# Kernel tuning notes

Hardware: AMD Instinct MI355X
Metric: run time of the kernel (lower is better)

The kernel has to match this reference:

```python
import jax, jax.numpy as jnp
import numpy as np

E = 256      # emb_size
H = 100      # ff_sim hidden
B, TQ, TK = 16, 128, 128


def setup_inputs() -> dict:
    key = jax.random.key(0)
    ks = jax.random.split(key, 8)
    queries = jax.random.normal(ks[0], (B, TQ, E), dtype=jnp.float32)
    keys = jax.random.normal(ks[1], (B, TK, E), dtype=jnp.float32)
    query_masks = jnp.ones((B, TQ), dtype=jnp.float32)
    key_masks = jnp.ones((B, TK), dtype=jnp.float32)
    # xavier_uniform bounds: sqrt(6/(fan_in+fan_out))
    def xavier(k, shape):
        fan_out, fan_in = shape
        lim = np.sqrt(6.0 / (fan_in + fan_out))
        return jax.random.uniform(k, shape, jnp.float32, -lim, lim)
    W1 = xavier(ks[2], (H, 2 * E))          # linear_ff_sim[0].weight
    b1 = jnp.zeros((H,), dtype=jnp.float32)  # linear_ff_sim[0].bias
    W2 = xavier(ks[3], (1, H))              # linear_ff_sim[2].weight (no bias)
    Wlast = xavier(ks[4], (E, 2 * E))       # linear_last.weight
    blast = jnp.zeros((E,), dtype=jnp.float32)
    return {"queries": queries, "keys": keys, "query_masks": query_masks,
            "key_masks": key_masks, "W1": W1, "b1": b1, "W2": W2,
            "Wlast": Wlast, "blast": blast}


def reference(queries, keys, query_masks, key_masks, W1, b1, W2, Wlast, blast):
    # forward calls attention_fc(keys, queries, key_masks, query_masks):
    #   attn queries = keys,  attn keys = queries,
    #   attn query_masks = key_masks, attn key_masks = query_masks.
    e = queries.shape[-1]
    # Additive-attention MLP score, decomposed: cat([keys_i, queries_j]) @ W1^T
    #   = keys_i @ W1[:, :E]^T + queries_j @ W1[:, E:]^T
    a = jnp.einsum('bie,he->bih', keys, W1[:, :e])      # [B,Tk,H]
    c = jnp.einsum('bje,he->bjh', queries, W1[:, e:])   # [B,Tq,H]
    h = jnp.tanh(a[:, :, None, :] + c[:, None, :, :] + b1)  # [B,Tk,Tq,H]
    sim = jnp.einsum('bijh,h->bij', h, W2[0])           # [B,Tk,Tq]
    neg = jnp.asarray(-2.0 ** 32 + 1, sim.dtype)
    sim = jnp.where(query_masks[:, None, :] == 0, neg, sim)
    sim = jax.nn.softmax(sim, axis=-1)
    sim = sim * key_masks[:, :, None]
    keys_attn = jnp.einsum('bij,bje->bie', sim, queries)  # [B,Tk,E]
    feature_mul = keys_attn * keys
    d = keys_attn - keys
    feature_sub = d * d
    feature_last = jnp.concatenate([feature_mul, feature_sub], axis=-1)  # [B,Tk,2E]
    return jax.nn.relu(jnp.einsum('bif,ef->bie', feature_last, Wlast) + blast)
```

## Files before the change

### kernel.cpp

```cpp
#include <hip/hip_runtime.h>


namespace {
constexpr int B  = 16;
constexpr int TQ = 128;
constexpr int TK = 128;
constexpr int E  = 256;
constexpr int H  = 100;
constexpr int HP = 112;
constexpr int G  = 4;
}

typedef __attribute__((ext_vector_type(8))) short short8;
typedef __attribute__((ext_vector_type(4))) float f32x4;

__device__ __forceinline__ unsigned short f2bf(float f) {
  unsigned u = __builtin_bit_cast(unsigned, f);
  u = (u + 0x7FFFu + ((u >> 16) & 1u)) >> 16;
  return (unsigned short)u;
}

__global__ __launch_bounds__(256) void convert_bf16(
    const float* __restrict__ queries, const float* __restrict__ keys,
    const float* __restrict__ W1, const float* __restrict__ Wlast,
    unsigned short* __restrict__ Xb, unsigned short* __restrict__ Wb1,
    unsigned short* __restrict__ Wb) {
  const int blk = blockIdx.x, t = threadIdx.x;
  if (blk < 1024) {
    const int idx = blk * 1024 + t * 4;
    const int row = idx >> 8, e = idx & 255;
    const float* src = (row < B * TK) ? keys + (size_t)row * E + e
                                      : queries + (size_t)(row - B * TK) * E + e;
    float4 v = *(const float4*)src;
    ushort4 o = make_ushort4(f2bf(v.x), f2bf(v.y), f2bf(v.z), f2bf(v.w));
    *(ushort4*)(Xb + idx) = o;
  } else if (blk < 1080) {
    const int idx = (blk - 1024) * 1024 + t * 4;
    const int h = idx >> 9;
    float4 v = (h < H) ? *(const float4*)(W1 + idx)
                       : make_float4(0.f, 0.f, 0.f, 0.f);
    ushort4 o = make_ushort4(f2bf(v.x), f2bf(v.y), f2bf(v.z), f2bf(v.w));
    *(ushort4*)(Wb1 + idx) = o;
  } else {
    const int idx = (blk - 1080) * 1024 + t * 4;
    float4 v = *(const float4*)(Wlast + idx);
    ushort4 o = make_ushort4(f2bf(v.x), f2bf(v.y), f2bf(v.z), f2bf(v.w));
    *(ushort4*)(Wb + idx) = o;
  }
}

__global__ __launch_bounds__(256) void prep_mfma(
    const unsigned short* __restrict__ Xb, const unsigned short* __restrict__ Wb1,
    const float* __restrict__ b1, float* __restrict__ A, float* __restrict__ C) {
  __shared__ short Bs[112 * 264];
  __shared__ short As[16 * 264];
  const int t  = threadIdx.x;
  const int m0 = blockIdx.x * 16;
  const bool isA = (m0 < B * TK);
  const int koff = isA ? 0 : 256;
  float* dst = isA ? (A + (size_t)m0 * HP)
                   : (C + (size_t)(m0 - B * TK) * HP);

  #pragma unroll
  for (int i = 0; i < 14; ++i) {
    const int idx = i * 256 + t;
    const int h = idx >> 5, seg = idx & 31;
    *(uint4*)(Bs + h * 264 + seg * 8) =
        *(const uint4*)(Wb1 + (size_t)h * 512 + koff + seg * 8);
  }
  #pragma unroll
  for (int i = 0; i < 2; ++i) {
    const int idx = i * 256 + t;
    const int r = idx >> 5, seg = idx & 31;
    *(uint4*)(As + r * 264 + seg * 8) =
        *(const uint4*)(Xb + (size_t)(m0 + r) * 256 + seg * 8);
  }
  __syncthreads();

  const int wave = t >> 6, lane = t & 63;
  const int m = lane & 15, kq = lane >> 4;
  const int nt0 = wave, nt1 = wave + 4;
  f32x4 acc0 = {0.f, 0.f, 0.f, 0.f}, acc1 = {0.f, 0.f, 0.f, 0.f};

  #pragma unroll
  for (int kc = 0; kc < 8; ++kc) {
    short8 a = *(const short8*)(As + m * 264 + kc * 32 + kq * 8);
    short8 bv0 = *(const short8*)(Bs + (nt0 * 16 + m) * 264 + kc * 32 + kq * 8);
    acc0 = __builtin_amdgcn_mfma_f32_16x16x32_bf16(a, bv0, acc0, 0, 0, 0);
    if (nt1 < 7) {
      short8 bv1 = *(const short8*)(Bs + (nt1 * 16 + m) * 264 + kc * 32 + kq * 8);
      acc1 = __builtin_amdgcn_mfma_f32_16x16x32_bf16(a, bv1, acc1, 0, 0, 0);
    }
  }

  const int rbase = (lane >> 4) * 4;
  {
    const int h = nt0 * 16 + m;
    const float bias = (isA && h < H) ? b1[h] : 0.0f;
    #pragma unroll
    for (int r = 0; r < 4; ++r)
      dst[(size_t)(rbase + r) * HP + h] = acc0[r] + bias;
  }
  if (nt1 < 7) {
    const int h = nt1 * 16 + m;
    const float bias = (isA && h < H) ? b1[h] : 0.0f;
    #pragma unroll
    for (int r = 0; r < 4; ++r)
      dst[(size_t)(rbase + r) * HP + h] = acc1[r] + bias;
  }
}

__global__ __launch_bounds__(512) void attn_core(
    const float* __restrict__ queries, const float* __restrict__ keys,
    const float* __restrict__ qmask, const float* __restrict__ kmask,
    const float* __restrict__ W2, const float* __restrict__ A,
    const float* __restrict__ C, unsigned short* __restrict__ feat ) {
  __shared__ float a_s[G * HP];
  __shared__ float w2s[HP];
  __shared__ float qm[TQ];
  __shared__ float simP[G * 512];
  __shared__ float pL[G * TQ];
  __shared__ float red[8];

  const int t   = threadIdx.x;
  const int blk = blockIdx.x;
  const int b   = blk >> 5;
  const int i0  = (blk & 31) * G;

  if (t < G * HP / 4)
    ((float4*)a_s)[t] = ((const float4*)(A + ((size_t)b * TK + i0) * HP))[t];
  if (t < HP) w2s[t] = (t < H) ? W2[t] : 0.0f;
  if (t < TQ) qm[t]  = qmask[b * TQ + t];
  __syncthreads();

  const int j = t & (TQ - 1);
  const int q = t >> 7;
  float4 cr[7], wr[7];
  float wsum = 0.0f;
  {
    const float4* c4 = (const float4*)(C + ((size_t)b * TQ + j) * HP + q * 28);
    const float4* w4 = (const float4*)w2s + q * 7;
    #pragma unroll
    for (int k = 0; k < 7; ++k) {
      cr[k] = c4[k];
      wr[k] = w4[k];
      wsum += wr[k].x + wr[k].y + wr[k].z + wr[k].w;
    }
  }
  {
    const float4* a4p = (const float4*)a_s + q * 7;
    #pragma unroll
    for (int g = 0; g < G; ++g) {
      float s = 0.0f;
      #pragma unroll
      for (int k = 0; k < 7; ++k) {
        float4 a4 = a4p[g * (HP / 4) + k];
        float x0 = a4.x + cr[k].x, x1 = a4.y + cr[k].y;
        float x2 = a4.z + cr[k].z, x3 = a4.w + cr[k].w;
        s = fmaf(wr[k].x, __builtin_amdgcn_rcpf(__expf(x0 + x0) + 1.0f), s);
        s = fmaf(wr[k].y, __builtin_amdgcn_rcpf(__expf(x1 + x1) + 1.0f), s);
        s = fmaf(wr[k].z, __builtin_amdgcn_rcpf(__expf(x2 + x2) + 1.0f), s);
        s = fmaf(wr[k].w, __builtin_amdgcn_rcpf(__expf(x3 + x3) + 1.0f), s);
      }
      simP[g * 512 + t] = wsum - 2.0f * s;
    }
  }
  __syncthreads();

  {
    const int g2 = t >> 7, j2 = t & 127;
    const float* sp = simP + g2 * 512 + j2;
    float sv = sp[0] + sp[128] + sp[256] + sp[384];
    if (qm[j2] == 0.0f) sv = -4294967295.0f;
    float p = __expf(sv);
    float s = p;
    #pragma unroll
    for (int off = 1; off < 64; off <<= 1) s += __shfl_xor(s, off, 64);
    if ((t & 63) == 0) red[t >> 6] = s;
    __syncthreads();
    pL[t] = p / (red[g2 * 2] + red[g2 * 2 + 1]);
  }
  __syncthreads();

  {
    const int e = t & 255, gh = t >> 8;
    float ka0 = 0.0f, ka1 = 0.0f;
    const float* qb = queries + (size_t)b * TQ * E + e;
    const float4* p4 = (const float4*)pL;
    for (int j4 = 0; j4 < TQ / 4; ++j4) {
      float4 p0 = p4[(gh * 2) * 32 + j4];
      float4 p1 = p4[(gh * 2 + 1) * 32 + j4];
      #pragma unroll
      for (int c = 0; c < 4; ++c) {
        float qv = qb[(size_t)(j4 * 4 + c) * E];
        ka0 = fmaf(((const float*)&p0)[c], qv, ka0);
        ka1 = fmaf(((const float*)&p1)[c], qv, ka1);
      }
    }
    #pragma unroll
    for (int gg = 0; gg < 2; ++gg) {
      const int g = gh * 2 + gg;
      const float ka = gg ? ka1 : ka0;
      const float kmv = kmask[b * TK + i0 + g];
      const float kav = ka * kmv;
      const float kv  = keys[((size_t)b * TK + i0 + g) * E + e];
      const size_t row = (size_t)(b * TK + i0 + g) * (2 * E);
      feat[row + e]     = f2bf(kav * kv);
      float d = kav - kv;
      feat[row + E + e] = f2bf(d * d);
    }
  }
}

__global__ __launch_bounds__(256) void last_gemm(
    const unsigned short* __restrict__ Wb ,
    const float* __restrict__ blast, float* __restrict__ out) {
  __shared__ short A_s[16 * 520];
  __shared__ short B_s[256 * 72];
  const int t  = threadIdx.x;
  const int m0 = blockIdx.x * 16;

  {
    const uint4* src = (const uint4*)out;
    #pragma unroll
    for (int i = 0; i < 4; ++i) {
      int idx = t + i * 256;
      int r = idx >> 6, c = idx & 63;
      *(uint4*)(A_s + r * 520 + c * 8) = src[(size_t)(m0 + r) * 64 + c];
    }
  }
  __syncthreads();

  f32x4 acc[4];
  #pragma unroll
  for (int nt = 0; nt < 4; ++nt) acc[nt] = f32x4{0.f, 0.f, 0.f, 0.f};

  const int wave = t >> 6, lane = t & 63;
  const int nsub = wave * 64;
  const int m    = lane & 15, kq = lane >> 4;

  for (int kc = 0; kc < 8; ++kc) {
    #pragma unroll
    for (int i = 0; i < 8; ++i) {
      int idx = t + i * 256;
      int r = idx >> 3, p = idx & 7;
      *(uint4*)(B_s + r * 72 + p * 8) =
          ((const uint4*)(Wb + (size_t)r * 512 + kc * 64))[p];
    }
    __syncthreads();
    #pragma unroll
    for (int ks = 0; ks < 2; ++ks) {
      short8 a = *(const short8*)(A_s + m * 520 + kc * 64 + ks * 32 + kq * 8);
      #pragma unroll
      for (int nt = 0; nt < 4; ++nt) {
        short8 bf = *(const short8*)(B_s + (nsub + nt * 16 + m) * 72 + ks * 32 + kq * 8);
        acc[nt] = __builtin_amdgcn_mfma_f32_16x16x32_bf16(a, bf, acc[nt], 0, 0, 0);
      }
    }
    __syncthreads();
  }

  const int col = lane & 15;
  const int rbase = m0 + (lane >> 4) * 4;
  #pragma unroll
  for (int nt = 0; nt < 4; ++nt) {
    const int e = nsub + nt * 16 + col;
    const float bl = blast[e];
    #pragma unroll
    for (int r = 0; r < 4; ++r)
      out[(size_t)(rbase + r) * 256 + e] = fmaxf(acc[nt][r] + bl, 0.0f);
  }
}

extern "C" void kernel_launch(void* const* d_in, const int* in_sizes, int n_in,
                              void* d_out, int out_size, void* d_ws, size_t ws_size,
                              hipStream_t stream) {
  (void)in_sizes; (void)n_in; (void)out_size; (void)ws_size;
  const float* queries = (const float*)d_in[0];
  const float* keys    = (const float*)d_in[1];
  const float* qmask   = (const float*)d_in[2];
  const float* kmask   = (const float*)d_in[3];
  const float* W1      = (const float*)d_in[4];
  const float* b1      = (const float*)d_in[5];
  const float* W2      = (const float*)d_in[6];
  const float* Wlast   = (const float*)d_in[7];
  const float* blast   = (const float*)d_in[8];
  float* out = (float*)d_out;

  float* A = (float*)d_ws;
  float* C = A + (size_t)B * TK * HP;
  unsigned short* Wb  = (unsigned short*)(C + (size_t)B * TQ * HP);
  unsigned short* Wb1 = Wb + (size_t)256 * 512;
  unsigned short* Xb  = Wb1 + (size_t)112 * 512;

  convert_bf16<<<dim3(1208), dim3(256), 0, stream>>>(
      queries, keys, W1, Wlast, Xb, Wb1, Wb);
  prep_mfma<<<dim3(256), dim3(256), 0, stream>>>(Xb, Wb1, b1, A, C);
  attn_core<<<dim3(B * (TK / G)), dim3(512), 0, stream>>>(
      queries, keys, qmask, kmask, W2, A, C, (unsigned short*)out);
  last_gemm<<<dim3(B * TK / 16), dim3(256), 0, stream>>>(Wb, blast, out);
}
```

Before: 101.0 us.

## Fuse bf16 conversion into prep and final GEMM into attention kernel

The separate bf16 conversion kernel is removed: W1 and the input rows are converted inline with packed cvt instructions while being loaded into shared memory, and a tail of extra prep blocks converts Wlast. The final linear layer moves into attn_core. Each block keeps its 4 feature rows in shared memory and runs MFMA directly against Wlast from global memory, which drops a launch and the feature round trip through memory. The tanh pre-activation is pre-scaled by 2/ln2 so a native exp2 can be used. The cost is that each block now reads the whole Wlast for only 4 useful rows of a 16-row MFMA, which multiplies weight traffic and wastes MFMA work.

```diff
diff --git a/kernel.cpp b/kernel.cpp
--- a/kernel.cpp
+++ b/kernel.cpp
@@ -9,6 +9,7 @@
 constexpr int H  = 100;
 constexpr int HP = 112;
 constexpr int G  = 4;
+constexpr float SCALE = 2.8853900817779268f;
 }
 
 typedef __attribute__((ext_vector_type(8))) short short8;
@@ -20,44 +21,40 @@
   return (unsigned short)u;
 }
 
-__global__ __launch_bounds__(256) void convert_bf16(
+__device__ __forceinline__ unsigned cvt_pk(float lo, float hi) {
+  unsigned r;
+  asm("v_cvt_pk_bf16_f32 %0, %1, %2" : "=v"(r) : "v"(lo), "v"(hi));
+  return r;
+}
+
+__device__ __forceinline__ uint4 cvt8(float4 v0, float4 v1) {
+  return make_uint4(cvt_pk(v0.x, v0.y), cvt_pk(v0.z, v0.w),
+                    cvt_pk(v1.x, v1.y), cvt_pk(v1.z, v1.w));
+}
+
+__global__ __launch_bounds__(256) void prep_mfma(
     const float* __restrict__ queries, const float* __restrict__ keys,
-    const float* __restrict__ W1, const float* __restrict__ Wlast,
-    unsigned short* __restrict__ Xb, unsigned short* __restrict__ Wb1,
+    const float* __restrict__ W1, const float* __restrict__ b1,
+    const float* __restrict__ Wlast,
+    float* __restrict__ A, float* __restrict__ C,
     unsigned short* __restrict__ Wb) {
-  const int blk = blockIdx.x, t = threadIdx.x;
-  if (blk < 1024) {
-    const int idx = blk * 1024 + t * 4;
-    const int row = idx >> 8, e = idx & 255;
-    const float* src = (row < B * TK) ? keys + (size_t)row * E + e
-                                      : queries + (size_t)(row - B * TK) * E + e;
-    float4 v = *(const float4*)src;
-    ushort4 o = make_ushort4(f2bf(v.x), f2bf(v.y), f2bf(v.z), f2bf(v.w));
-    *(ushort4*)(Xb + idx) = o;
-  } else if (blk < 1080) {
-    const int idx = (blk - 1024) * 1024 + t * 4;
-    const int h = idx >> 9;
-    float4 v = (h < H) ? *(const float4*)(W1 + idx)
-                       : make_float4(0.f, 0.f, 0.f, 0.f);
-    ushort4 o = make_ushort4(f2bf(v.x), f2bf(v.y), f2bf(v.z), f2bf(v.w));
-    *(ushort4*)(Wb1 + idx) = o;
-  } else {
-    const int idx = (blk - 1080) * 1024 + t * 4;
-    float4 v = *(const float4*)(Wlast + idx);
-    ushort4 o = make_ushort4(f2bf(v.x), f2bf(v.y), f2bf(v.z), f2bf(v.w));
-    *(ushort4*)(Wb + idx) = o;
-  }
-}
-
-__global__ __launch_bounds__(256) void prep_mfma(
-    const unsigned short* __restrict__ Xb, const unsigned short* __restrict__ Wb1,
-    const float* __restrict__ b1, float* __restrict__ A, float* __restrict__ C) {
+  const int t = threadIdx.x;
+
+  if (blockIdx.x >= 256) {
+    const int idx = ((blockIdx.x - 256) * 256 + t) * 8;
+    float4 v0 = *(const float4*)(Wlast + idx);
+    float4 v1 = *(const float4*)(Wlast + idx + 4);
+    *(uint4*)(Wb + idx) = cvt8(v0, v1);
+    return;
+  }
+
   __shared__ short Bs[112 * 264];
   __shared__ short As[16 * 264];
-  const int t  = threadIdx.x;
   const int m0 = blockIdx.x * 16;
   const bool isA = (m0 < B * TK);
   const int koff = isA ? 0 : 256;
+  const float* Xsrc = isA ? keys + (size_t)m0 * E
+                          : queries + (size_t)(m0 - B * TK) * E;
   float* dst = isA ? (A + (size_t)m0 * HP)
                    : (C + (size_t)(m0 - B * TK) * HP);
 
@@ -65,15 +62,22 @@
   for (int i = 0; i < 14; ++i) {
     const int idx = i * 256 + t;
     const int h = idx >> 5, seg = idx & 31;
-    *(uint4*)(Bs + h * 264 + seg * 8) =
-        *(const uint4*)(Wb1 + (size_t)h * 512 + koff + seg * 8);
+    uint4 o;
+    if (h < H) {
+      const float* s = W1 + (size_t)h * 512 + koff + seg * 8;
+      o = cvt8(*(const float4*)s, *(const float4*)(s + 4));
+    } else {
+      o = make_uint4(0u, 0u, 0u, 0u);
+    }
+    *(uint4*)(Bs + h * 264 + seg * 8) = o;
   }
   #pragma unroll
   for (int i = 0; i < 2; ++i) {
     const int idx = i * 256 + t;
     const int r = idx >> 5, seg = idx & 31;
-    *(uint4*)(As + r * 264 + seg * 8) =
-        *(const uint4*)(Xb + (size_t)(m0 + r) * 256 + seg * 8);
+    const float* s = Xsrc + (size_t)r * E + seg * 8;
+    *(uint4*)(As + r * 264 + seg * 8) = cvt8(*(const float4*)s,
+                                             *(const float4*)(s + 4));
   }
   __syncthreads();
 
@@ -99,14 +103,14 @@
     const float bias = (isA && h < H) ? b1[h] : 0.0f;
     #pragma unroll
     for (int r = 0; r < 4; ++r)
-      dst[(size_t)(rbase + r) * HP + h] = acc0[r] + bias;
+      dst[(size_t)(rbase + r) * HP + h] = (acc0[r] + bias) * SCALE;
   }
   if (nt1 < 7) {
     const int h = nt1 * 16 + m;
     const float bias = (isA && h < H) ? b1[h] : 0.0f;
     #pragma unroll
     for (int r = 0; r < 4; ++r)
-      dst[(size_t)(rbase + r) * HP + h] = acc1[r] + bias;
+      dst[(size_t)(rbase + r) * HP + h] = (acc1[r] + bias) * SCALE;
   }
 }
 
@@ -114,13 +118,15 @@
     const float* __restrict__ queries, const float* __restrict__ keys,
     const float* __restrict__ qmask, const float* __restrict__ kmask,
     const float* __restrict__ W2, const float* __restrict__ A,
-    const float* __restrict__ C, unsigned short* __restrict__ feat ) {
+    const float* __restrict__ C, const unsigned short* __restrict__ Wb,
+    const float* __restrict__ blast, float* __restrict__ out) {
   __shared__ float a_s[G * HP];
   __shared__ float w2s[HP];
   __shared__ float qm[TQ];
   __shared__ float simP[G * 512];
   __shared__ float pL[G * TQ];
   __shared__ float red[8];
+  __shared__ short feat_s[16 * 520];
 
   const int t   = threadIdx.x;
   const int blk = blockIdx.x;
@@ -157,10 +163,10 @@
         float4 a4 = a4p[g * (HP / 4) + k];
         float x0 = a4.x + cr[k].x, x1 = a4.y + cr[k].y;
         float x2 = a4.z + cr[k].z, x3 = a4.w + cr[k].w;
-        s = fmaf(wr[k].x, __builtin_amdgcn_rcpf(__expf(x0 + x0) + 1.0f), s);
-        s = fmaf(wr[k].y, __builtin_amdgcn_rcpf(__expf(x1 + x1) + 1.0f), s);
-        s = fmaf(wr[k].z, __builtin_amdgcn_rcpf(__expf(x2 + x2) + 1.0f), s);
-        s = fmaf(wr[k].w, __builtin_amdgcn_rcpf(__expf(x3 + x3) + 1.0f), s);
+        s = fmaf(wr[k].x, __builtin_amdgcn_rcpf(__builtin_amdgcn_exp2f(x0) + 1.0f), s);
+        s = fmaf(wr[k].y, __builtin_amdgcn_rcpf(__builtin_amdgcn_exp2f(x1) + 1.0f), s);
+        s = fmaf(wr[k].z, __builtin_amdgcn_rcpf(__builtin_amdgcn_exp2f(x2) + 1.0f), s);
+        s = fmaf(wr[k].w, __builtin_amdgcn_rcpf(__builtin_amdgcn_exp2f(x3) + 1.0f), s);
       }
       simP[g * 512 + t] = wsum - 2.0f * s;
     }
@@ -204,71 +210,39 @@
       const float kmv = kmask[b * TK + i0 + g];
       const float kav = ka * kmv;
       const float kv  = keys[((size_t)b * TK + i0 + g) * E + e];
-      const size_t row = (size_t)(b * TK + i0 + g) * (2 * E);
-      feat[row + e]     = f2bf(kav * kv);
+      feat_s[g * 520 + e]     = (short)f2bf(kav * kv);
       float d = kav - kv;
-      feat[row + E + e] = f2bf(d * d);
-    }
-  }
-}
-
-__global__ __launch_bounds__(256) void last_gemm(
-    const unsigned short* __restrict__ Wb ,
-    const float* __restrict__ blast, float* __restrict__ out) {
-  __shared__ short A_s[16 * 520];
-  __shared__ short B_s[256 * 72];
-  const int t  = threadIdx.x;
-  const int m0 = blockIdx.x * 16;
-
-  {
-    const uint4* src = (const uint4*)out;
-    #pragma unroll
-    for (int i = 0; i < 4; ++i) {
-      int idx = t + i * 256;
-      int r = idx >> 6, c = idx & 63;
-      *(uint4*)(A_s + r * 520 + c * 8) = src[(size_t)(m0 + r) * 64 + c];
-    }
-  }
-  __syncthreads();
-
-  f32x4 acc[4];
-  #pragma unroll
-  for (int nt = 0; nt < 4; ++nt) acc[nt] = f32x4{0.f, 0.f, 0.f, 0.f};
-
-  const int wave = t >> 6, lane = t & 63;
-  const int nsub = wave * 64;
-  const int m    = lane & 15, kq = lane >> 4;
-
-  for (int kc = 0; kc < 8; ++kc) {
-    #pragma unroll
-    for (int i = 0; i < 8; ++i) {
-      int idx = t + i * 256;
-      int r = idx >> 3, p = idx & 7;
-      *(uint4*)(B_s + r * 72 + p * 8) =
-          ((const uint4*)(Wb + (size_t)r * 512 + kc * 64))[p];
-    }
-    __syncthreads();
-    #pragma unroll
-    for (int ks = 0; ks < 2; ++ks) {
-      short8 a = *(const short8*)(A_s + m * 520 + kc * 64 + ks * 32 + kq * 8);
+      feat_s[g * 520 + E + e] = (short)f2bf(d * d);
+    }
+  }
+  __syncthreads();
+
+  {
+    const int wave = t >> 6, lane = t & 63;
+    const int nsub = wave * 32;
+    const int m = lane & 15, kq = lane >> 4;
+    f32x4 acc0 = {0.f, 0.f, 0.f, 0.f}, acc1 = {0.f, 0.f, 0.f, 0.f};
+    const unsigned short* wb0 = Wb + (size_t)(nsub + m) * 512 + kq * 8;
+    const unsigned short* wb1 = wb0 + (size_t)16 * 512;
+    const short* ap = feat_s + m * 520 + kq * 8;
+    #pragma unroll
+    for (int ks = 0; ks < 16; ++ks) {
+      short8 a  = *(const short8*)(ap + ks * 32);
+      short8 b0 = *(const short8*)(wb0 + ks * 32);
+      acc0 = __builtin_amdgcn_mfma_f32_16x16x32_bf16(a, b0, acc0, 0, 0, 0);
+      short8 b1v = *(const short8*)(wb1 + ks * 32);
+      acc1 = __builtin_amdgcn_mfma_f32_16x16x32_bf16(a, b1v, acc1, 0, 0, 0);
+    }
+    if (lane < 16) {
+      const size_t row0 = (size_t)(b * TK + i0) * 256;
+      const int e0 = nsub + lane, e1 = nsub + 16 + lane;
+      const float bl0 = blast[e0], bl1 = blast[e1];
       #pragma unroll
-      for (int nt = 0; nt < 4; ++nt) {
-        short8 bf = *(const short8*)(B_s + (nsub + nt * 16 + m) * 72 + ks * 32 + kq * 8);
-        acc[nt] = __builtin_amdgcn_mfma_f32_16x16x32_bf16(a, bf, acc[nt], 0, 0, 0);
+      for (int r = 0; r < 4; ++r) {
+        out[row0 + (size_t)r * 256 + e0] = fmaxf(acc0[r] + bl0, 0.0f);
+        out[row0 + (size_t)r * 256 + e1] = fmaxf(acc1[r] + bl1, 0.0f);
       }
     }
-    __syncthreads();
-  }
-
-  const int col = lane & 15;
-  const int rbase = m0 + (lane >> 4) * 4;
-  #pragma unroll
-  for (int nt = 0; nt < 4; ++nt) {
-    const int e = nsub + nt * 16 + col;
-    const float bl = blast[e];
-    #pragma unroll
-    for (int r = 0; r < 4; ++r)
-      out[(size_t)(rbase + r) * 256 + e] = fmaxf(acc[nt][r] + bl, 0.0f);
   }
 }
 
@@ -289,14 +263,10 @@
 
   float* A = (float*)d_ws;
   float* C = A + (size_t)B * TK * HP;
-  unsigned short* Wb  = (unsigned short*)(C + (size_t)B * TQ * HP);
-  unsigned short* Wb1 = Wb + (size_t)256 * 512;
-  unsigned short* Xb  = Wb1 + (size_t)112 * 512;
-
-  convert_bf16<<<dim3(1208), dim3(256), 0, stream>>>(
-      queries, keys, W1, Wlast, Xb, Wb1, Wb);
-  prep_mfma<<<dim3(256), dim3(256), 0, stream>>>(Xb, Wb1, b1, A, C);
+  unsigned short* Wb = (unsigned short*)(C + (size_t)B * TQ * HP);
+
+  prep_mfma<<<dim3(320), dim3(256), 0, stream>>>(
+      queries, keys, W1, b1, Wlast, A, C, Wb);
   attn_core<<<dim3(B * (TK / G)), dim3(512), 0, stream>>>(
-      queries, keys, qmask, kmask, W2, A, C, (unsigned short*)out);
-  last_gemm<<<dim3(B * TK / 16), dim3(256), 0, stream>>>(Wb, blast, out);
-}
+      queries, keys, qmask, kmask, W2, A, C, Wb, blast, out);
+}
```

Result: no change. 101.3 us (+0.3%).
